# Kernel tuning notes

Measured on AMD Instinct MI355X. Metric: run time of the kernel, lower is better.

Reference implementation:

```python
import jax, jax.numpy as jnp
import numpy as np

N = 50000
IN, HID, OUT, HEADS = 128, 64, 64, 4


def seg_softmax(logits, seg, num):
    # softmax over edges grouped by destination node; logits [E, H]
    m = jax.ops.segment_max(logits, seg, num_segments=num)
    e = jnp.exp(logits - m[seg])
    s = jax.ops.segment_sum(e, seg, num_segments=num)
    return e / (s[seg] + 1e-16)


def gat_conv(x, src, dst, W, a_s, a_d, b, heads, concat):
    n = x.shape[0]
    h = (x @ W.T).reshape(n, heads, -1)           # [N, H, C]
    alpha_src = jnp.einsum('nhc,hc->nh', h, a_s)   # per-node src score
    alpha_dst = jnp.einsum('nhc,hc->nh', h, a_d)
    logits = jax.nn.leaky_relu(alpha_src[src] + alpha_dst[dst], 0.2)  # [E, H]
    alpha = seg_softmax(logits, dst, n)
    out = jax.ops.segment_sum(alpha[:, :, None] * h[src], dst, num_segments=n)  # [N, H, C]
    out = out.reshape(n, -1) if concat else out.mean(axis=1)
    return out + b


def setup_inputs():
    key = jax.random.key(0)
    ks = jax.random.split(key, 16)
    x = jax.random.normal(ks[0], (N, IN), dtype=jnp.float32)
    edge_index = jax.random.randint(ks[1], (2, 800000), 0, N, dtype=jnp.int64)

    def glorot(k, shape):
        fan = shape[-1]
        return jax.random.normal(k, shape, dtype=jnp.float32) / jnp.sqrt(jnp.float32(fan))

    d = {"x": x, "edge_index": edge_index}
    # layer 1: IN -> HID, HEADS heads, concat
    d["W1"] = glorot(ks[2], (HEADS * HID, IN))
    d["as1"] = glorot(ks[3], (HEADS, HID))
    d["ad1"] = glorot(ks[4], (HEADS, HID))
    d["b1"] = jnp.zeros((HEADS * HID,), jnp.float32)
    # layer 2: HID*HEADS -> HID, HEADS heads, concat
    d["W2"] = glorot(ks[5], (HEADS * HID, HEADS * HID))
    d["as2"] = glorot(ks[6], (HEADS, HID))
    d["ad2"] = glorot(ks[7], (HEADS, HID))
    d["b2"] = jnp.zeros((HEADS * HID,), jnp.float32)
    # layer 3: HID*HEADS -> OUT, 1 head
    d["W3"] = glorot(ks[8], (OUT, HEADS * HID))
    d["as3"] = glorot(ks[9], (1, OUT))
    d["ad3"] = glorot(ks[10], (1, OUT))
    d["b3"] = jnp.zeros((OUT,), jnp.float32)
    return d


def reference(x, edge_index, W1, as1, ad1, b1, W2, as2, ad2, b2, W3, as3, ad3, b3):
    # PyG GATConv adds self-loops by default
    loops = jnp.arange(N, dtype=edge_index.dtype)
    src = jnp.concatenate([edge_index[0], loops])
    dst = jnp.concatenate([edge_index[1], loops])

    h = jax.nn.relu(gat_conv(x, src, dst, W1, as1, ad1, b1, HEADS, True))
    h = jax.nn.relu(gat_conv(h, src, dst, W2, as2, ad2, b2, HEADS, True))
    out = gat_conv(h, src, dst, W3, as3, ad3, b3, 1, True)
    return out
```

## Files before the change

### kernel.cpp

```cpp
#include <hip/hip_runtime.h>
#include <hip/hip_bf16.h>
#include <math.h>


typedef __bf16 bf16x8 __attribute__((ext_vector_type(8)));
typedef float f32x4 __attribute__((ext_vector_type(4)));

#define QINV 2048.0f
#define QDQ  4.8828125e-4f

__device__ __forceinline__ void gload_lds16(const void* g, void* l) {
  __builtin_amdgcn_global_load_lds(
      (const __attribute__((address_space(1))) unsigned int*)g,
      (__attribute__((address_space(3))) unsigned int*)l, 16, 0, 0);
}

__device__ __forceinline__ unsigned int splitf(float a) {
  __hip_bfloat16 h = __float2bfloat16(a);
  float hf = __bfloat162float(h);
  __hip_bfloat16 l = __float2bfloat16(a - hf);
  return (unsigned int)__builtin_bit_cast(unsigned short, h) |
         ((unsigned int)__builtin_bit_cast(unsigned short, l) << 16);
}

__device__ __forceinline__ float leaky02(float l) {
  return (l >= 0.f) ? l : 0.2f * l;
}

__device__ __forceinline__ short quant16(float v) {
  int q = (int)rintf(v * QINV);
  q = q > 32767 ? 32767 : (q < -32768 ? -32768 : q);
  return (short)q;
}


__global__ void init_counts_kernel(int* counts, int n) {
  int i = blockIdx.x * blockDim.x + threadIdx.x;
  if (i < n) counts[i] = 1;
}

__global__ void hist_kernel(const int* __restrict__ dst, int e, int* counts) {
  int i = blockIdx.x * blockDim.x + threadIdx.x;
  if (i < e) atomicAdd(&counts[dst[i]], 1);
}

__global__ __launch_bounds__(1024) void block_sum_kernel(const int* __restrict__ counts,
                                                         int* __restrict__ bsum, int n) {
  __shared__ int red[1024];
  int i = blockIdx.x * 1024 + threadIdx.x;
  red[threadIdx.x] = (i < n) ? counts[i] : 0;
  __syncthreads();
  #pragma unroll
  for (int off = 512; off > 0; off >>= 1) {
    if (threadIdx.x < off) red[threadIdx.x] += red[threadIdx.x + off];
    __syncthreads();
  }
  if (threadIdx.x == 0) bsum[blockIdx.x] = red[0];
}

__global__ void scan_sums_kernel(int* bsum, int nb) {
  int t = threadIdx.x;
  int c = (t < nb) ? bsum[t] : 0;
  int v = c;
  #pragma unroll
  for (int off = 1; off < 64; off <<= 1) {
    int u = __shfl_up(v, off);
    if (t >= off) v += u;
  }
  if (t < nb) bsum[t] = v - c;
}

__global__ __launch_bounds__(1024) void scan_final_kernel(const int* __restrict__ counts,
    const int* __restrict__ bsum, int* __restrict__ offsets, int* __restrict__ cursor, int n) {
  __shared__ int sc[1024];
  int i = blockIdx.x * 1024 + threadIdx.x;
  int c = (i < n) ? counts[i] : 0;
  sc[threadIdx.x] = c;
  __syncthreads();
  for (int off = 1; off < 1024; off <<= 1) {
    int v = 0;
    if (threadIdx.x >= off) v = sc[threadIdx.x - off];
    __syncthreads();
    sc[threadIdx.x] += v;
    __syncthreads();
  }
  int excl = sc[threadIdx.x] - c + bsum[blockIdx.x];
  if (i < n) {
    offsets[i] = excl;
    cursor[i] = excl;
  } else if (i == n) {
    offsets[n] = excl;
  }
}

__global__ void scatter_kernel(const int* __restrict__ src, const int* __restrict__ dst,
                               int e800, int etot, int* cursor, int* __restrict__ ssrc) {
  int i = blockIdx.x * blockDim.x + threadIdx.x;
  if (i >= etot) return;
  int s, d;
  if (i < e800) { s = src[i]; d = dst[i]; }
  else          { s = i - e800; d = s; }
  int pos = atomicAdd(&cursor[d], 1);
  ssrc[pos] = s;
}

__global__ void split_kernel(const float* __restrict__ in, uint4* __restrict__ out, int count4) {
  int i = blockIdx.x * blockDim.x + threadIdx.x;
  if (i >= count4) return;
  float4 v = reinterpret_cast<const float4*>(in)[i];
  uint4 o;
  o.x = splitf(v.x); o.y = splitf(v.y); o.z = splitf(v.z); o.w = splitf(v.w);
  out[i] = o;
}

template <int KP, int BM, int BN, int WAVES_M, int WAVES_N, int OTOT>
__global__ __launch_bounds__(256) void gemm2_kernel(
    const unsigned short* __restrict__ A, const unsigned short* __restrict__ B,
    short* __restrict__ Cq, int M) {
  constexpr int BK = 64;
  constexpr int NK = KP / BK;
  constexpr int MFRAG = BM / WAVES_M / 16;
  constexpr int NFRAG = BN / WAVES_N / 16;
  __shared__ unsigned short As[2][BM * BK];
  __shared__ unsigned short Bs[2][BN * BK];

  const int tid = threadIdx.x;
  const int lane = tid & 63;
  const int wid = tid >> 6;
  const int m0 = blockIdx.x * BM;
  const int o0 = blockIdx.y * BN;

  const int srow = tid >> 3;
  const int scolb = (tid & 7) * 16;
  const int sswz = (srow & 7) << 4;
  const char* aSrc = (const char*)A + (size_t)(m0 + srow) * (KP * 2) + (scolb ^ sswz);
  const char* bSrc = (const char*)B + (size_t)(o0 + srow) * (KP * 2) + (scolb ^ sswz);
  char* aDst0 = (char*)&As[0][0] + wid * 1024;
  char* bDst0 = (char*)&Bs[0][0] + wid * 1024;

  auto stage = [&](int buf, int kt) {
    const size_t ko = (size_t)kt * 128;
    char* ad = aDst0 + buf * (BM * 128);
    #pragma unroll
    for (int i = 0; i < BM / 32; ++i)
      gload_lds16(aSrc + ko + (size_t)i * 32 * (KP * 2), ad + i * 4096);
    char* bd = bDst0 + buf * (BN * 128);
    #pragma unroll
    for (int j = 0; j < BN / 32; ++j)
      gload_lds16(bSrc + ko + (size_t)j * 32 * (KP * 2), bd + j * 4096);
  };

  const int fr = lane & 15;
  const int fg = lane >> 4;
  const int fswz = (fr & 7) << 4;
  const int wm0 = (wid / WAVES_N) * (BM / WAVES_M);
  const int wn0 = (wid % WAVES_N) * (BN / WAVES_N);

  f32x4 acc[MFRAG][NFRAG];
  #pragma unroll
  for (int mi = 0; mi < MFRAG; ++mi)
    #pragma unroll
    for (int ni = 0; ni < NFRAG; ++ni) acc[mi][ni] = (f32x4)0.f;

  stage(0, 0);
  __syncthreads();

  for (int kt = 0; kt < NK; ++kt) {
    const int buf = kt & 1;
    if (kt + 1 < NK) stage(buf ^ 1, kt + 1);
    const char* asB = (const char*)&As[buf][0] + (wm0 + fr) * 128;
    const char* bsB = (const char*)&Bs[buf][0] + (wn0 + fr) * 128;
    #pragma unroll
    for (int kh = 0; kh < 2; ++kh) {
      const int kb = (kh * 64 + fg * 16) ^ fswz;
      bf16x8 af[MFRAG], bfr[NFRAG];
      #pragma unroll
      for (int mi = 0; mi < MFRAG; ++mi)
        af[mi] = *reinterpret_cast<const bf16x8*>(asB + mi * 16 * 128 + kb);
      #pragma unroll
      for (int ni = 0; ni < NFRAG; ++ni)
        bfr[ni] = *reinterpret_cast<const bf16x8*>(bsB + ni * 16 * 128 + kb);
      #pragma unroll
      for (int mi = 0; mi < MFRAG; ++mi)
        #pragma unroll
        for (int ni = 0; ni < NFRAG; ++ni)
          acc[mi][ni] = __builtin_amdgcn_mfma_f32_16x16x32_bf16(af[mi], bfr[ni], acc[mi][ni], 0, 0, 0);
    }
    __syncthreads();
  }

  #pragma unroll
  for (int mi = 0; mi < MFRAG; ++mi) {
    #pragma unroll
    for (int r = 0; r < 4; ++r) {
      int row = m0 + wm0 + mi * 16 + fg * 4 + r;
      if (row < M) {
        #pragma unroll
        for (int ni = 0; ni < NFRAG; ++ni)
          Cq[(size_t)row * OTOT + o0 + wn0 + ni * 16 + fr] = quant16(acc[mi][ni][r]);
      }
    }
  }
}

__global__ __launch_bounds__(256) void alpha4_kernel(const short* __restrict__ hq,
    const float* __restrict__ a_s, const float* __restrict__ a_d,
    float* __restrict__ asrc, float* __restrict__ adst, int n) {
  int wid = threadIdx.x >> 6;
  int lane = threadIdx.x & 63;
  int node = blockIdx.x * 4 + wid;
  if (node >= n) return;
  short4 q = *reinterpret_cast<const short4*>(&hq[(size_t)node * 256 + lane * 4]);
  float4 sv = *reinterpret_cast<const float4*>(&a_s[lane * 4]);
  float4 dv = *reinterpret_cast<const float4*>(&a_d[lane * 4]);
  float h0 = (float)q.x, h1 = (float)q.y, h2 = (float)q.z, h3 = (float)q.w;
  float ps = h0 * sv.x + h1 * sv.y + h2 * sv.z + h3 * sv.w;
  float pd = h0 * dv.x + h1 * dv.y + h2 * dv.z + h3 * dv.w;
  #pragma unroll
  for (int off = 1; off < 16; off <<= 1) {
    ps += __shfl_xor(ps, off);
    pd += __shfl_xor(pd, off);
  }
  if ((lane & 15) == 0) {
    int head = lane >> 4;
    asrc[node * 4 + head] = ps * QDQ;
    adst[node * 4 + head] = pd * QDQ;
  }
}

__global__ __launch_bounds__(256) void alpha1_kernel(const short* __restrict__ hq,
    const float* __restrict__ a_s, const float* __restrict__ a_d,
    float* __restrict__ asrc, float* __restrict__ adst, int n) {
  int wid = threadIdx.x >> 6;
  int lane = threadIdx.x & 63;
  int node = blockIdx.x * 4 + wid;
  if (node >= n) return;
  float hv = (float)hq[(size_t)node * 64 + lane];
  float ps = hv * a_s[lane];
  float pd = hv * a_d[lane];
  #pragma unroll
  for (int off = 1; off < 64; off <<= 1) {
    ps += __shfl_xor(ps, off);
    pd += __shfl_xor(pd, off);
  }
  if (lane == 0) { asrc[node] = ps * QDQ; adst[node] = pd * QDQ; }
}

template <bool RELU, bool SPLIT>
__global__ __launch_bounds__(256) void aggregate4_kernel(
    const short* __restrict__ hq, const float* __restrict__ asrc,
    const float* __restrict__ adst, const float* __restrict__ bias,
    const int* __restrict__ offsets, const int* __restrict__ ssrc,
    void* __restrict__ outp, int n) {
  int wid = threadIdx.x >> 6;
  int lane = threadIdx.x & 63;
  int node = blockIdx.x * 4 + wid;
  if (node >= n) return;
  int head = lane >> 4;
  float adv = adst[(size_t)node * 4 + head];
  int beg = offsets[node], end = offsets[node + 1];

  float s0 = 0.f, s1 = 0.f, s2 = 0.f, s3 = 0.f;
  float4 A0 = {0, 0, 0, 0}, A1 = {0, 0, 0, 0}, A2 = {0, 0, 0, 0}, A3 = {0, 0, 0, 0};
  int e = beg;
  for (; e + 3 < end; e += 4) {
    int c0 = ssrc[e + 0], c1 = ssrc[e + 1], c2 = ssrc[e + 2], c3 = ssrc[e + 3];
    float p0 = __expf(leaky02(asrc[(size_t)c0 * 4 + head] + adv));
    float p1 = __expf(leaky02(asrc[(size_t)c1 * 4 + head] + adv));
    float p2 = __expf(leaky02(asrc[(size_t)c2 * 4 + head] + adv));
    float p3 = __expf(leaky02(asrc[(size_t)c3 * 4 + head] + adv));
    short4 q0 = *reinterpret_cast<const short4*>(&hq[(size_t)c0 * 256 + lane * 4]);
    short4 q1 = *reinterpret_cast<const short4*>(&hq[(size_t)c1 * 256 + lane * 4]);
    short4 q2 = *reinterpret_cast<const short4*>(&hq[(size_t)c2 * 256 + lane * 4]);
    short4 q3 = *reinterpret_cast<const short4*>(&hq[(size_t)c3 * 256 + lane * 4]);
    s0 += p0; s1 += p1; s2 += p2; s3 += p3;
    A0.x += p0 * (float)q0.x; A0.y += p0 * (float)q0.y; A0.z += p0 * (float)q0.z; A0.w += p0 * (float)q0.w;
    A1.x += p1 * (float)q1.x; A1.y += p1 * (float)q1.y; A1.z += p1 * (float)q1.z; A1.w += p1 * (float)q1.w;
    A2.x += p2 * (float)q2.x; A2.y += p2 * (float)q2.y; A2.z += p2 * (float)q2.z; A2.w += p2 * (float)q2.w;
    A3.x += p3 * (float)q3.x; A3.y += p3 * (float)q3.y; A3.z += p3 * (float)q3.z; A3.w += p3 * (float)q3.w;
  }
  for (; e < end; ++e) {
    int c0 = ssrc[e];
    float p0 = __expf(leaky02(asrc[(size_t)c0 * 4 + head] + adv));
    short4 q0 = *reinterpret_cast<const short4*>(&hq[(size_t)c0 * 256 + lane * 4]);
    s0 += p0;
    A0.x += p0 * (float)q0.x; A0.y += p0 * (float)q0.y; A0.z += p0 * (float)q0.z; A0.w += p0 * (float)q0.w;
  }
  float s = (s0 + s1) + (s2 + s3);
  float4 A;
  A.x = (A0.x + A1.x) + (A2.x + A3.x);
  A.y = (A0.y + A1.y) + (A2.y + A3.y);
  A.z = (A0.z + A1.z) + (A2.z + A3.z);
  A.w = (A0.w + A1.w) + (A2.w + A3.w);

  float inv = QDQ / (s + 1e-16f);
  float4 bv = *reinterpret_cast<const float4*>(&bias[lane * 4]);
  float4 o;
  o.x = A.x * inv + bv.x;
  o.y = A.y * inv + bv.y;
  o.z = A.z * inv + bv.z;
  o.w = A.w * inv + bv.w;
  if (RELU) {
    o.x = fmaxf(o.x, 0.f); o.y = fmaxf(o.y, 0.f);
    o.z = fmaxf(o.z, 0.f); o.w = fmaxf(o.w, 0.f);
  }
  if (SPLIT) {
    uint4 pk;
    pk.x = splitf(o.x); pk.y = splitf(o.y); pk.z = splitf(o.z); pk.w = splitf(o.w);
    reinterpret_cast<uint4*>(outp)[(size_t)node * 64 + lane] = pk;
  } else {
    reinterpret_cast<float4*>(outp)[(size_t)node * 64 + lane] = o;
  }
}

__global__ __launch_bounds__(256) void aggregate1_kernel(
    const short* __restrict__ hq, const float* __restrict__ asrc,
    const float* __restrict__ adst, const float* __restrict__ bias,
    const int* __restrict__ offsets, const int* __restrict__ ssrc,
    float* __restrict__ out, int n) {
  int wid = threadIdx.x >> 6;
  int lane = threadIdx.x & 63;
  int node = blockIdx.x * 4 + wid;
  if (node >= n) return;
  int g = lane >> 4;
  int w = lane & 15;
  float adv = adst[node];
  int beg = offsets[node], end = offsets[node + 1];

  float s = 0.f;
  float4 A = {0, 0, 0, 0};
  int e0 = beg;
  for (; e0 + 3 < end; e0 += 4) {
    int src = ssrc[e0 + g];
    float p = __expf(leaky02(asrc[src] + adv));
    short4 q = *reinterpret_cast<const short4*>(&hq[(size_t)src * 64 + w * 4]);
    s += p;
    A.x += p * (float)q.x; A.y += p * (float)q.y;
    A.z += p * (float)q.z; A.w += p * (float)q.w;
  }
  if (e0 + g < end) {
    int src = ssrc[e0 + g];
    float p = __expf(leaky02(asrc[src] + adv));
    short4 q = *reinterpret_cast<const short4*>(&hq[(size_t)src * 64 + w * 4]);
    s += p;
    A.x += p * (float)q.x; A.y += p * (float)q.y;
    A.z += p * (float)q.z; A.w += p * (float)q.w;
  }
  #pragma unroll
  for (int off = 16; off < 64; off <<= 1) {
    s += __shfl_xor(s, off);
    A.x += __shfl_xor(A.x, off);
    A.y += __shfl_xor(A.y, off);
    A.z += __shfl_xor(A.z, off);
    A.w += __shfl_xor(A.w, off);
  }
  if (g == 0) {
    float inv = QDQ / (s + 1e-16f);
    float4 bv = *reinterpret_cast<const float4*>(&bias[w * 4]);
    float4 o;
    o.x = A.x * inv + bv.x;
    o.y = A.y * inv + bv.y;
    o.z = A.z * inv + bv.z;
    o.w = A.w * inv + bv.w;
    *reinterpret_cast<float4*>(&out[(size_t)node * 64 + w * 4]) = o;
  }
}


extern "C" void kernel_launch(void* const* d_in, const int* in_sizes, int n_in,
                              void* d_out, int out_size, void* d_ws, size_t ws_size,
                              hipStream_t stream) {
  const float* x   = (const float*)d_in[0];
  const int*   ei  = (const int*)d_in[1];
  const float* W1  = (const float*)d_in[2];
  const float* as1 = (const float*)d_in[3];
  const float* ad1 = (const float*)d_in[4];
  const float* b1  = (const float*)d_in[5];
  const float* W2  = (const float*)d_in[6];
  const float* as2 = (const float*)d_in[7];
  const float* ad2 = (const float*)d_in[8];
  const float* b2  = (const float*)d_in[9];
  const float* W3  = (const float*)d_in[10];
  const float* as3 = (const float*)d_in[11];
  const float* ad3 = (const float*)d_in[12];
  const float* b3  = (const float*)d_in[13];
  float* out = (float*)d_out;

  const int n    = in_sizes[0] / 128;
  const int e800 = in_sizes[1] / 2;
  const int etot = e800 + n;
  const int Mpad = 50048;

  char* ws = (char*)d_ws;
  size_t off = 0;
  auto alloc = [&](size_t bytes) -> void* {
    void* p = ws + off;
    off = (off + bytes + 255) & ~(size_t)255;
    return p;
  };
  short*          featQ  = (short*)alloc((size_t)Mpad * 256 * 2);
  unsigned short* hsplit = (unsigned short*)alloc((size_t)Mpad * 512 * 2);
  unsigned short* w1s    = (unsigned short*)alloc((size_t)256 * 256 * 2);
  unsigned short* w2s    = (unsigned short*)alloc((size_t)256 * 512 * 2);
  unsigned short* w3s    = (unsigned short*)alloc((size_t)64 * 512 * 2);
  float* asrc    = (float*)alloc((size_t)n * 4 * 4);
  float* adst    = (float*)alloc((size_t)n * 4 * 4);
  int*   ssrc    = (int*)alloc((size_t)etot * 4);
  int*   offsets = (int*)alloc((size_t)(n + 1) * 4);
  int*   cursor  = (int*)alloc((size_t)n * 4);
  int*   counts  = (int*)alloc((size_t)n * 4);
  int*   bsum    = (int*)alloc((size_t)64 * 4);

  const int* esrc = ei;
  const int* edst = ei + e800;
  const int nbScan = (n + 1024) / 1024;

  init_counts_kernel<<<(n + 255) / 256, 256, 0, stream>>>(counts, n);
  hist_kernel<<<(e800 + 255) / 256, 256, 0, stream>>>(edst, e800, counts);
  block_sum_kernel<<<nbScan, 1024, 0, stream>>>(counts, bsum, n);
  scan_sums_kernel<<<1, 64, 0, stream>>>(bsum, nbScan);
  scan_final_kernel<<<nbScan, 1024, 0, stream>>>(counts, bsum, offsets, cursor, n);
  scatter_kernel<<<(etot + 255) / 256, 256, 0, stream>>>(esrc, edst, e800, etot, cursor, ssrc);

  split_kernel<<<(n * 128 / 4 + 255) / 256, 256, 0, stream>>>(x, (uint4*)hsplit, n * 128 / 4);
  split_kernel<<<(256 * 128 / 4 + 255) / 256, 256, 0, stream>>>(W1, (uint4*)w1s, 256 * 128 / 4);
  split_kernel<<<(256 * 256 / 4 + 255) / 256, 256, 0, stream>>>(W2, (uint4*)w2s, 256 * 256 / 4);
  split_kernel<<<(64 * 256 / 4 + 255) / 256, 256, 0, stream>>>(W3, (uint4*)w3s, 64 * 256 / 4);

  const int nodeBlocks = (n + 3) / 4;
  const int mBlocks = Mpad / 128;

  gemm2_kernel<256, 128, 128, 2, 2, 256><<<dim3(mBlocks, 2), 256, 0, stream>>>(hsplit, w1s, featQ, n);
  alpha4_kernel<<<nodeBlocks, 256, 0, stream>>>(featQ, as1, ad1, asrc, adst, n);
  aggregate4_kernel<true, true><<<nodeBlocks, 256, 0, stream>>>(featQ, asrc, adst, b1, offsets, ssrc, hsplit, n);

  gemm2_kernel<512, 128, 128, 2, 2, 256><<<dim3(mBlocks, 2), 256, 0, stream>>>(hsplit, w2s, featQ, n);
  alpha4_kernel<<<nodeBlocks, 256, 0, stream>>>(featQ, as2, ad2, asrc, adst, n);
  aggregate4_kernel<true, true><<<nodeBlocks, 256, 0, stream>>>(featQ, asrc, adst, b2, offsets, ssrc, hsplit, n);

  gemm2_kernel<512, 128, 64, 4, 1, 64><<<dim3(mBlocks, 1), 256, 0, stream>>>(hsplit, w3s, featQ, n);
  alpha1_kernel<<<nodeBlocks, 256, 0, stream>>>(featQ, as3, ad3, asrc, adst, n);
  aggregate1_kernel<<<nodeBlocks, 256, 0, stream>>>(featQ, asrc, adst, b3, offsets, ssrc, out, n);
}
```

Baseline: 373.2 us.

## Fuse attention-score computation into GEMM epilogue and switch features to fp16

```diff
diff --git a/kernel.cpp b/kernel.cpp
--- a/kernel.cpp
+++ b/kernel.cpp
@@ -5,6 +5,7 @@
 
 typedef __bf16 bf16x8 __attribute__((ext_vector_type(8)));
 typedef float f32x4 __attribute__((ext_vector_type(4)));
+typedef _Float16 half8v __attribute__((ext_vector_type(8)));
 
 #define QINV 2048.0f
 #define QDQ  4.8828125e-4f
@@ -113,10 +114,28 @@
   out[i] = o;
 }
 
-template <int KP, int BM, int BN, int WAVES_M, int WAVES_N, int OTOT>
+__global__ void splitW_kernel(const float* __restrict__ W1, const float* __restrict__ W2,
+                              const float* __restrict__ W3, uint4* __restrict__ o1,
+                              uint4* __restrict__ o2, uint4* __restrict__ o3) {
+  int i = blockIdx.x * blockDim.x + threadIdx.x;
+  const float* in;
+  uint4* out;
+  int j;
+  if (i < 8192)            { in = W1; out = o1; j = i; }
+  else if (i < 8192+16384) { in = W2; out = o2; j = i - 8192; }
+  else if (i < 8192+16384+4096) { in = W3; out = o3; j = i - (8192+16384); }
+  else return;
+  float4 v = reinterpret_cast<const float4*>(in)[j];
+  uint4 o;
+  o.x = splitf(v.x); o.y = splitf(v.y); o.z = splitf(v.z); o.w = splitf(v.w);
+  out[j] = o;
+}
+
+template <int KP, int BM, int BN, int WAVES_M, int WAVES_N, int OTOT, int HEADS, bool FP16OUT>
 __global__ __launch_bounds__(256) void gemm2_kernel(
     const unsigned short* __restrict__ A, const unsigned short* __restrict__ B,
-    short* __restrict__ Cq, int M) {
+    void* __restrict__ Cq, const float* __restrict__ a_s, const float* __restrict__ a_d,
+    float* __restrict__ asrcO, float* __restrict__ adstO, int M) {
   constexpr int BK = 64;
   constexpr int NK = KP / BK;
   constexpr int MFRAG = BM / WAVES_M / 16;
@@ -189,128 +208,89 @@
     __syncthreads();
   }
 
+  const int head = (o0 + wn0) >> 6;
+  float asl[NFRAG], adl[NFRAG];
+  #pragma unroll
+  for (int ni = 0; ni < NFRAG; ++ni) {
+    int c64 = ni * 16 + fr;
+    asl[ni] = a_s[head * 64 + c64];
+    adl[ni] = a_d[head * 64 + c64];
+  }
   #pragma unroll
   for (int mi = 0; mi < MFRAG; ++mi) {
     #pragma unroll
     for (int r = 0; r < 4; ++r) {
       int row = m0 + wm0 + mi * 16 + fg * 4 + r;
+      float ps = 0.f, pd = 0.f;
+      #pragma unroll
+      for (int ni = 0; ni < NFRAG; ++ni) {
+        ps = fmaf(acc[mi][ni][r], asl[ni], ps);
+        pd = fmaf(acc[mi][ni][r], adl[ni], pd);
+      }
+      #pragma unroll
+      for (int off = 1; off < 16; off <<= 1) {
+        ps += __shfl_xor(ps, off);
+        pd += __shfl_xor(pd, off);
+      }
       if (row < M) {
+        if (fr == 0) {
+          asrcO[(size_t)row * HEADS + head] = ps;
+          adstO[(size_t)row * HEADS + head] = pd;
+        }
         #pragma unroll
-        for (int ni = 0; ni < NFRAG; ++ni)
-          Cq[(size_t)row * OTOT + o0 + wn0 + ni * 16 + fr] = quant16(acc[mi][ni][r]);
+        for (int ni = 0; ni < NFRAG; ++ni) {
+          size_t ci = (size_t)row * OTOT + o0 + wn0 + ni * 16 + fr;
+          if (FP16OUT) ((_Float16*)Cq)[ci] = (_Float16)acc[mi][ni][r];
+          else         ((short*)Cq)[ci] = quant16(acc[mi][ni][r]);
+        }
       }
     }
   }
 }
 
-__global__ __launch_bounds__(256) void alpha4_kernel(const short* __restrict__ hq,
-    const float* __restrict__ a_s, const float* __restrict__ a_d,
-    float* __restrict__ asrc, float* __restrict__ adst, int n) {
+__global__ __launch_bounds__(256) void aggregate4_kernel(
+    const _Float16* __restrict__ hq, const float* __restrict__ asrc,
+    const float* __restrict__ adst, const float* __restrict__ bias,
+    const int* __restrict__ offsets, const int* __restrict__ ssrc,
+    uint4* __restrict__ outp, int n) {
   int wid = threadIdx.x >> 6;
   int lane = threadIdx.x & 63;
-  int node = blockIdx.x * 4 + wid;
+  int sub = lane >> 5;
+  int hl = lane & 31;
+  int node = blockIdx.x * 8 + wid * 2 + sub;
   if (node >= n) return;
-  short4 q = *reinterpret_cast<const short4*>(&hq[(size_t)node * 256 + lane * 4]);
-  float4 sv = *reinterpret_cast<const float4*>(&a_s[lane * 4]);
-  float4 dv = *reinterpret_cast<const float4*>(&a_d[lane * 4]);
-  float h0 = (float)q.x, h1 = (float)q.y, h2 = (float)q.z, h3 = (float)q.w;
-  float ps = h0 * sv.x + h1 * sv.y + h2 * sv.z + h3 * sv.w;
-  float pd = h0 * dv.x + h1 * dv.y + h2 * dv.z + h3 * dv.w;
-  #pragma unroll
-  for (int off = 1; off < 16; off <<= 1) {
-    ps += __shfl_xor(ps, off);
-    pd += __shfl_xor(pd, off);
-  }
-  if ((lane & 15) == 0) {
-    int head = lane >> 4;
-    asrc[node * 4 + head] = ps * QDQ;
-    adst[node * 4 + head] = pd * QDQ;
-  }
-}
-
-__global__ __launch_bounds__(256) void alpha1_kernel(const short* __restrict__ hq,
-    const float* __restrict__ a_s, const float* __restrict__ a_d,
-    float* __restrict__ asrc, float* __restrict__ adst, int n) {
-  int wid = threadIdx.x >> 6;
-  int lane = threadIdx.x & 63;
-  int node = blockIdx.x * 4 + wid;
-  if (node >= n) return;
-  float hv = (float)hq[(size_t)node * 64 + lane];
-  float ps = hv * a_s[lane];
-  float pd = hv * a_d[lane];
-  #pragma unroll
-  for (int off = 1; off < 64; off <<= 1) {
-    ps += __shfl_xor(ps, off);
-    pd += __shfl_xor(pd, off);
-  }
-  if (lane == 0) { asrc[node] = ps * QDQ; adst[node] = pd * QDQ; }
-}
-
-template <bool RELU, bool SPLIT>
-__global__ __launch_bounds__(256) void aggregate4_kernel(
-    const short* __restrict__ hq, const float* __restrict__ asrc,
-    const float* __restrict__ adst, const float* __restrict__ bias,
-    const int* __restrict__ offsets, const int* __restrict__ ssrc,
-    void* __restrict__ outp, int n) {
-  int wid = threadIdx.x >> 6;
-  int lane = threadIdx.x & 63;
-  int node = blockIdx.x * 4 + wid;
-  if (node >= n) return;
-  int head = lane >> 4;
+  int head = hl >> 3;
+  int ch8 = hl * 8;
   float adv = adst[(size_t)node * 4 + head];
   int beg = offsets[node], end = offsets[node + 1];
 
-  float s0 = 0.f, s1 = 0.f, s2 = 0.f, s3 = 0.f;
-  float4 A0 = {0, 0, 0, 0}, A1 = {0, 0, 0, 0}, A2 = {0, 0, 0, 0}, A3 = {0, 0, 0, 0};
-  int e = beg;
-  for (; e + 3 < end; e += 4) {
-    int c0 = ssrc[e + 0], c1 = ssrc[e + 1], c2 = ssrc[e + 2], c3 = ssrc[e + 3];
-    float p0 = __expf(leaky02(asrc[(size_t)c0 * 4 + head] + adv));
-    float p1 = __expf(leaky02(asrc[(size_t)c1 * 4 + head] + adv));
-    float p2 = __expf(leaky02(asrc[(size_t)c2 * 4 + head] + adv));
-    float p3 = __expf(leaky02(asrc[(size_t)c3 * 4 + head] + adv));
-    short4 q0 = *reinterpret_cast<const short4*>(&hq[(size_t)c0 * 256 + lane * 4]);
-    short4 q1 = *reinterpret_cast<const short4*>(&hq[(size_t)c1 * 256 + lane * 4]);
-    short4 q2 = *reinterpret_cast<const short4*>(&hq[(size_t)c2 * 256 + lane * 4]);
-    short4 q3 = *reinterpret_cast<const short4*>(&hq[(size_t)c3 * 256 + lane * 4]);
-    s0 += p0; s1 += p1; s2 += p2; s3 += p3;
-    A0.x += p0 * (float)q0.x; A0.y += p0 * (float)q0.y; A0.z += p0 * (float)q0.z; A0.w += p0 * (float)q0.w;
-    A1.x += p1 * (float)q1.x; A1.y += p1 * (float)q1.y; A1.z += p1 * (float)q1.z; A1.w += p1 * (float)q1.w;
-    A2.x += p2 * (float)q2.x; A2.y += p2 * (float)q2.y; A2.z += p2 * (float)q2.z; A2.w += p2 * (float)q2.w;
-    A3.x += p3 * (float)q3.x; A3.y += p3 * (float)q3.y; A3.z += p3 * (float)q3.z; A3.w += p3 * (float)q3.w;
-  }
-  for (; e < end; ++e) {
-    int c0 = ssrc[e];
-    float p0 = __expf(leaky02(asrc[(size_t)c0 * 4 + head] + adv));
-    short4 q0 = *reinterpret_cast<const short4*>(&hq[(size_t)c0 * 256 + lane * 4]);
-    s0 += p0;
-    A0.x += p0 * (float)q0.x; A0.y += p0 * (float)q0.y; A0.z += p0 * (float)q0.z; A0.w += p0 * (float)q0.w;
-  }
-  float s = (s0 + s1) + (s2 + s3);
-  float4 A;
-  A.x = (A0.x + A1.x) + (A2.x + A3.x);
-  A.y = (A0.y + A1.y) + (A2.y + A3.y);
-  A.z = (A0.z + A1.z) + (A2.z + A3.z);
-  A.w = (A0.w + A1.w) + (A2.w + A3.w);
-
-  float inv = QDQ / (s + 1e-16f);
-  float4 bv = *reinterpret_cast<const float4*>(&bias[lane * 4]);
-  float4 o;
-  o.x = A.x * inv + bv.x;
-  o.y = A.y * inv + bv.y;
-  o.z = A.z * inv + bv.z;
-  o.w = A.w * inv + bv.w;
-  if (RELU) {
-    o.x = fmaxf(o.x, 0.f); o.y = fmaxf(o.y, 0.f);
-    o.z = fmaxf(o.z, 0.f); o.w = fmaxf(o.w, 0.f);
-  }
-  if (SPLIT) {
-    uint4 pk;
-    pk.x = splitf(o.x); pk.y = splitf(o.y); pk.z = splitf(o.z); pk.w = splitf(o.w);
-    reinterpret_cast<uint4*>(outp)[(size_t)node * 64 + lane] = pk;
-  } else {
-    reinterpret_cast<float4*>(outp)[(size_t)node * 64 + lane] = o;
-  }
+  float s = 0.f;
+  float A[8] = {};
+  for (int e = beg; e < end; ++e) {
+    int c = ssrc[e];
+    float p = __expf(leaky02(asrc[(size_t)c * 4 + head] + adv));
+    half8v hv = *reinterpret_cast<const half8v*>(&hq[(size_t)c * 256 + ch8]);
+    s += p;
+    #pragma unroll
+    for (int j = 0; j < 8; ++j) A[j] = fmaf((float)hv[j], p, A[j]);
+  }
+  float inv = 1.f / (s + 1e-16f);
+  float4 bv0 = *reinterpret_cast<const float4*>(&bias[ch8]);
+  float4 bv1 = *reinterpret_cast<const float4*>(&bias[ch8 + 4]);
+  float o[8];
+  o[0] = fmaxf(A[0] * inv + bv0.x, 0.f);
+  o[1] = fmaxf(A[1] * inv + bv0.y, 0.f);
+  o[2] = fmaxf(A[2] * inv + bv0.z, 0.f);
+  o[3] = fmaxf(A[3] * inv + bv0.w, 0.f);
+  o[4] = fmaxf(A[4] * inv + bv1.x, 0.f);
+  o[5] = fmaxf(A[5] * inv + bv1.y, 0.f);
+  o[6] = fmaxf(A[6] * inv + bv1.z, 0.f);
+  o[7] = fmaxf(A[7] * inv + bv1.w, 0.f);
+  uint4 pk0, pk1;
+  pk0.x = splitf(o[0]); pk0.y = splitf(o[1]); pk0.z = splitf(o[2]); pk0.w = splitf(o[3]);
+  pk1.x = splitf(o[4]); pk1.y = splitf(o[5]); pk1.z = splitf(o[6]); pk1.w = splitf(o[7]);
+  outp[(size_t)node * 64 + hl * 2 + 0] = pk0;
+  outp[(size_t)node * 64 + hl * 2 + 1] = pk1;
 }
 
 __global__ __launch_bounds__(256) void aggregate1_kernel(
@@ -398,7 +378,7 @@
     off = (off + bytes + 255) & ~(size_t)255;
     return p;
   };
-  short*          featQ  = (short*)alloc((size_t)Mpad * 256 * 2);
+  void*           featQ  = alloc((size_t)Mpad * 256 * 2);
   unsigned short* hsplit = (unsigned short*)alloc((size_t)Mpad * 512 * 2);
   unsigned short* w1s    = (unsigned short*)alloc((size_t)256 * 256 * 2);
   unsigned short* w2s    = (unsigned short*)alloc((size_t)256 * 512 * 2);
@@ -423,22 +403,23 @@
   scatter_kernel<<<(etot + 255) / 256, 256, 0, stream>>>(esrc, edst, e800, etot, cursor, ssrc);
 
   split_kernel<<<(n * 128 / 4 + 255) / 256, 256, 0, stream>>>(x, (uint4*)hsplit, n * 128 / 4);
-  split_kernel<<<(256 * 128 / 4 + 255) / 256, 256, 0, stream>>>(W1, (uint4*)w1s, 256 * 128 / 4);
-  split_kernel<<<(256 * 256 / 4 + 255) / 256, 256, 0, stream>>>(W2, (uint4*)w2s, 256 * 256 / 4);
-  split_kernel<<<(64 * 256 / 4 + 255) / 256, 256, 0, stream>>>(W3, (uint4*)w3s, 64 * 256 / 4);
-
-  const int nodeBlocks = (n + 3) / 4;
+  splitW_kernel<<<(8192 + 16384 + 4096 + 255) / 256, 256, 0, stream>>>(
+      W1, W2, W3, (uint4*)w1s, (uint4*)w2s, (uint4*)w3s);
+
   const int mBlocks = Mpad / 128;
 
-  gemm2_kernel<256, 128, 128, 2, 2, 256><<<dim3(mBlocks, 2), 256, 0, stream>>>(hsplit, w1s, featQ, n);
-  alpha4_kernel<<<nodeBlocks, 256, 0, stream>>>(featQ, as1, ad1, asrc, adst, n);
-  aggregate4_kernel<true, true><<<nodeBlocks, 256, 0, stream>>>(featQ, asrc, adst, b1, offsets, ssrc, hsplit, n);
-
-  gemm2_kernel<512, 128, 128, 2, 2, 256><<<dim3(mBlocks, 2), 256, 0, stream>>>(hsplit, w2s, featQ, n);
-  alpha4_kernel<<<nodeBlocks, 256, 0, stream>>>(featQ, as2, ad2, asrc, adst, n);
-  aggregate4_kernel<true, true><<<nodeBlocks, 256, 0, stream>>>(featQ, asrc, adst, b2, offsets, ssrc, hsplit, n);
-
-  gemm2_kernel<512, 128, 64, 4, 1, 64><<<dim3(mBlocks, 1), 256, 0, stream>>>(hsplit, w3s, featQ, n);
-  alpha1_kernel<<<nodeBlocks, 256, 0, stream>>>(featQ, as3, ad3, asrc, adst, n);
-  aggregate1_kernel<<<nodeBlocks, 256, 0, stream>>>(featQ, asrc, adst, b3, offsets, ssrc, out, n);
-}
+  gemm2_kernel<256, 128, 128, 2, 2, 256, 4, true><<<dim3(mBlocks, 2), 256, 0, stream>>>(
+      hsplit, w1s, featQ, as1, ad1, asrc, adst, n);
+  aggregate4_kernel<<<(n + 7) / 8, 256, 0, stream>>>(
+      (const _Float16*)featQ, asrc, adst, b1, offsets, ssrc, (uint4*)hsplit, n);
+
+  gemm2_kernel<512, 128, 128, 2, 2, 256, 4, true><<<dim3(mBlocks, 2), 256, 0, stream>>>(
+      hsplit, w2s, featQ, as2, ad2, asrc, adst, n);
+  aggregate4_kernel<<<(n + 7) / 8, 256, 0, stream>>>(
+      (const _Float16*)featQ, asrc, adst, b2, offsets, ssrc, (uint4*)hsplit, n);
+
+  gemm2_kernel<512, 128, 64, 4, 1, 64, 1, false><<<dim3(mBlocks, 1), 256, 0, stream>>>(
+      hsplit, w3s, featQ, as3, ad3, asrc, adst, n);
+  aggregate1_kernel<<<(n + 3) / 4, 256, 0, stream>>>(
+      (const short*)featQ, asrc, adst, b3, offsets, ssrc, out, n);
+}
```

Measured after the change: 374.5 us. Within noise of the previous version (+0.3%).
